# Optimization experiments

Hardware: AMD Instinct MI355X
Metric: run time of the kernel (lower is better)

## Reference

```python
import jax, jax.numpy as jnp
import numpy as np

L = 32768
D_MODEL = 1024
D_HIDDEN = 1024


def setup_inputs() -> dict:
    key = jax.random.key(0)
    k_in, k_lam, k_B, k_C, k_D = jax.random.split(key, 5)
    inputs = jax.random.normal(k_in, (L, D_MODEL), dtype=jnp.float32)
    # uniform_init(normalization=sqrt(d_model)): U(-1,1)/sqrt(d_model) -> |lambda|<1, stable recurrence
    diag_lambda = jax.random.uniform(k_lam, (D_HIDDEN,), dtype=jnp.float32, minval=-1.0, maxval=1.0) / jnp.sqrt(float(D_MODEL))
    B = jax.random.normal(k_B, (D_HIDDEN, D_MODEL), dtype=jnp.float32) / jnp.sqrt(float(D_MODEL))
    C = jax.random.normal(k_C, (D_MODEL, D_HIDDEN), dtype=jnp.float32) / jnp.sqrt(float(D_HIDDEN))
    D = jax.random.normal(k_D, (D_MODEL,), dtype=jnp.float32)
    return {"inputs": inputs, "diag_lambda": diag_lambda, "B": B, "C": C, "D": D}


def _binop_diag(q_i, q_j):
    # elementwise diagonal linear-recurrence combine: (A, b) o (A', b') = (A'*A, A'*b + b')
    A_i, b_i = q_i
    A_j, b_j = q_j
    return (A_j * A_i, A_j * b_i + b_j)


def reference(inputs, diag_lambda, B, C, D):
    # h_t = lambda * h_{t-1} + B x_t ; y_t = C h_t + D * x_t
    Bu = jnp.einsum('ld,hd->lh', inputs, B)                     # [L, d_hidden]
    Lam = jnp.broadcast_to(diag_lambda[None, :], Bu.shape)      # [L, d_hidden]
    _, hidden = jax.lax.associative_scan(_binop_diag, (Lam, Bu))
    outputs = jnp.einsum('lh,dh->ld', hidden, C) + D[None, :] * inputs
    return outputs
```

## Files before the change

### kernel.cpp

```cpp
#include <hip/hip_runtime.h>

#define L_SEQ   32768
#define DMODEL  1024
#define DHIDDEN 1024
#define CHS     64
#define NCHS    (L_SEQ / CHS)
#define HALO    12

using f32x4  = __attribute__((ext_vector_type(4))) float;
using bf16x8 = __attribute__((ext_vector_type(8))) short;

typedef __attribute__((address_space(3))) unsigned char lds_byte_t;
typedef __attribute__((address_space(1))) const unsigned char glb_byte_t;

__device__ __forceinline__ void gld_lds16(const void* g, void* l) {
    __builtin_amdgcn_global_load_lds((glb_byte_t*)g, (lds_byte_t*)l, 16, 0, 0);
}

__device__ __forceinline__ unsigned short f2bf(float x) {
    unsigned u = __float_as_uint(x);
    unsigned r = u + 0x7fffu + ((u >> 16) & 1u);
    return (unsigned short)(r >> 16);
}
__device__ __forceinline__ float bf2f(unsigned short h) {
    return __uint_as_float(((unsigned)h) << 16);
}
__device__ __forceinline__ void split2(float x, unsigned short& hi, unsigned short& lo) {
    hi = f2bf(x);
    lo = f2bf(x - bf2f(hi));
}

__global__ __launch_bounds__(256)
void split_kernel(const float* __restrict__ in, unsigned short* __restrict__ hi,
                  unsigned short* __restrict__ lo, int n4)
{
    int i = blockIdx.x * 256 + threadIdx.x;
    const int stride = gridDim.x * 256;
    for (; i < n4; i += stride) {
        float4 v = ((const float4*)in)[i];
        ushort4 h, l;
        split2(v.x, h.x, l.x);
        split2(v.y, h.y, l.y);
        split2(v.z, h.z, l.z);
        split2(v.w, h.w, l.w);
        ((ushort4*)hi)[i] = h;
        ((ushort4*)lo)[i] = l;
    }
}

template<int EPI>
__global__ __launch_bounds__(256, 2)
void gemm3_bt(const unsigned short* __restrict__ Ahi, const unsigned short* __restrict__ Alo,
              const unsigned short* __restrict__ Bthi, const unsigned short* __restrict__ Btlo,
              int M, int N, int K,
              float* __restrict__ outF,
              const float* __restrict__ Dv, const float* __restrict__ X)
{
    __shared__ __align__(16) unsigned short smem[2][16384];

    const int tid  = threadIdx.x;
    const int wave = tid >> 6;
    const int lane = tid & 63;

    const int nbn = N >> 7;
    const int nwg = gridDim.x;
    const int cpx = nwg >> 3;
    const int swz = (blockIdx.x & 7) * cpx + (blockIdx.x >> 3);
    const int bm = swz / nbn, bn = swz % nbn;
    const int m0 = bm << 7, n0 = bn << 7;

    const int wr = wave >> 1, wc = wave & 1;

    const unsigned short* plane = (wave == 0) ? Ahi : (wave == 1) ? Alo
                                 : (wave == 2) ? Bthi : Btlo;
    const int r0 = (wave < 2) ? m0 : n0;

    const unsigned short* src0; const unsigned short* src1;
    const unsigned short* src2; const unsigned short* src3;
    const unsigned short* src4; const unsigned short* src5;
    const unsigned short* src6; const unsigned short* src7;
    int lo0, lo1, lo2, lo3, lo4, lo5, lo6, lo7;
    {
        const unsigned short* sp[8];
        int lofs[8];
#pragma unroll
        for (int i = 0; i < 8; ++i) {
            const int c   = i * 64 + lane;
            const int kg  = c >> 7;
            const int row = c & 127;
            sp[i]   = plane + (size_t)(r0 + row) * K + kg * 8;
            lofs[i] = wave * 4096 + c * 8;
        }
        src0 = sp[0]; src1 = sp[1]; src2 = sp[2]; src3 = sp[3];
        src4 = sp[4]; src5 = sp[5]; src6 = sp[6]; src7 = sp[7];
        lo0 = lofs[0]; lo1 = lofs[1]; lo2 = lofs[2]; lo3 = lofs[3];
        lo4 = lofs[4]; lo5 = lofs[5]; lo6 = lofs[6]; lo7 = lofs[7];
    }

#define STAGE(BUF, KOFF)                                                    \
    do {                                                                    \
        gld_lds16(src0 + (KOFF), &smem[BUF][lo0]);                          \
        gld_lds16(src1 + (KOFF), &smem[BUF][lo1]);                          \
        gld_lds16(src2 + (KOFF), &smem[BUF][lo2]);                          \
        gld_lds16(src3 + (KOFF), &smem[BUF][lo3]);                          \
        gld_lds16(src4 + (KOFF), &smem[BUF][lo4]);                          \
        gld_lds16(src5 + (KOFF), &smem[BUF][lo5]);                          \
        gld_lds16(src6 + (KOFF), &smem[BUF][lo6]);                          \
        gld_lds16(src7 + (KOFF), &smem[BUF][lo7]);                          \
    } while (0)

    f32x4 acc[4][4] = {};
    const int kgL = lane >> 4;
    const int rL  = lane & 15;

#define COMPUTE(BUF)                                                        \
    do {                                                                    \
        const unsigned short* sc = smem[BUF];                               \
        bf16x8 ah[4], al[4], bh[4], bl[4];                                  \
        _Pragma("unroll")                                                   \
        for (int mi = 0; mi < 4; ++mi) {                                    \
            const int off = kgL * 1024 + (wr * 64 + mi * 16 + rL) * 8;      \
            ah[mi] = *(const bf16x8*)&sc[off];                              \
            al[mi] = *(const bf16x8*)&sc[4096 + off];                       \
        }                                                                   \
        _Pragma("unroll")                                                   \
        for (int ni = 0; ni < 4; ++ni) {                                    \
            const int off = kgL * 1024 + (wc * 64 + ni * 16 + rL) * 8;      \
            bh[ni] = *(const bf16x8*)&sc[8192 + off];                       \
            bl[ni] = *(const bf16x8*)&sc[12288 + off];                      \
        }                                                                   \
        _Pragma("unroll")                                                   \
        for (int mi = 0; mi < 4; ++mi)                                      \
            _Pragma("unroll")                                               \
            for (int ni = 0; ni < 4; ++ni) {                                \
                acc[mi][ni] = __builtin_amdgcn_mfma_f32_16x16x32_bf16(      \
                    ah[mi], bh[ni], acc[mi][ni], 0, 0, 0);                  \
                acc[mi][ni] = __builtin_amdgcn_mfma_f32_16x16x32_bf16(      \
                    ah[mi], bl[ni], acc[mi][ni], 0, 0, 0);                  \
                acc[mi][ni] = __builtin_amdgcn_mfma_f32_16x16x32_bf16(      \
                    al[mi], bh[ni], acc[mi][ni], 0, 0, 0);                  \
            }                                                               \
    } while (0)

    STAGE(0, 0);
    __syncthreads();

    for (int k0 = 0; k0 < K; k0 += 64) {
        STAGE(1, k0 + 32);
        COMPUTE(0);
        __syncthreads();
        if (k0 + 64 < K) STAGE(0, k0 + 64);
        COMPUTE(1);
        __syncthreads();
    }
#undef STAGE
#undef COMPUTE

    const int orow = (lane >> 4) * 4;
    const int ocol = lane & 15;
#pragma unroll
    for (int mi = 0; mi < 4; ++mi)
#pragma unroll
        for (int ni = 0; ni < 4; ++ni)
#pragma unroll
            for (int r = 0; r < 4; ++r) {
                const int row = m0 + wr * 64 + mi * 16 + orow + r;
                const int col = n0 + wc * 64 + ni * 16 + ocol;
                float v = acc[mi][ni][r];
                if (EPI)
                    v = fmaf(Dv[col], X[(size_t)row * N + col], v);
                outF[(size_t)row * N + col] = v;
            }
}

__global__ __launch_bounds__(256)
void scan_fused(const float* __restrict__ Bu, const float* __restrict__ lam,
                unsigned short* __restrict__ Hhi, unsigned short* __restrict__ Hlo)
{
    const int c  = blockIdx.x;
    const int h0 = threadIdx.x * 4;
    float4 l4 = *(const float4*)&lam[h0];
    float hx = 0.f, hy = 0.f, hz = 0.f, hw = 0.f;

    const int r0 = c * CHS;
    const int hs = (c == 0) ? 0 : HALO;
    const float* p = Bu + (size_t)(r0 - hs) * DHIDDEN + h0;

    for (int r = 0; r < hs; ++r) {
        float4 v = *(const float4*)p;
        hx = fmaf(l4.x, hx, v.x);
        hy = fmaf(l4.y, hy, v.y);
        hz = fmaf(l4.z, hz, v.z);
        hw = fmaf(l4.w, hw, v.w);
        p += DHIDDEN;
    }

    unsigned short* ph = Hhi + (size_t)r0 * DHIDDEN + h0;
    unsigned short* pl = Hlo + (size_t)r0 * DHIDDEN + h0;
    for (int r = 0; r < CHS; ++r) {
        float4 v = *(const float4*)p;
        hx = fmaf(l4.x, hx, v.x);
        hy = fmaf(l4.y, hy, v.y);
        hz = fmaf(l4.z, hz, v.z);
        hw = fmaf(l4.w, hw, v.w);
        ushort4 oh, ol;
        split2(hx, oh.x, ol.x);
        split2(hy, oh.y, ol.y);
        split2(hz, oh.z, ol.z);
        split2(hw, oh.w, ol.w);
        *(ushort4*)ph = oh;
        *(ushort4*)pl = ol;
        p  += DHIDDEN;
        ph += DHIDDEN;
        pl += DHIDDEN;
    }
}

extern "C" void kernel_launch(void* const* d_in, const int* in_sizes, int n_in,
                              void* d_out, int out_size, void* d_ws, size_t ws_size,
                              hipStream_t stream)
{
    const float* X   = (const float*)d_in[0];
    const float* lam = (const float*)d_in[1];
    const float* B   = (const float*)d_in[2];
    const float* C   = (const float*)d_in[3];
    const float* Dv  = (const float*)d_in[4];
    float* out = (float*)d_out;

    unsigned short* Xhi = (unsigned short*)d_out;
    unsigned short* Xlo = Xhi + (size_t)L_SEQ * DMODEL;

    float* Bu = (float*)d_ws;
    unsigned short* Hhi = (unsigned short*)(Bu + (size_t)L_SEQ * DHIDDEN);
    unsigned short* Hlo = Hhi + (size_t)L_SEQ * DHIDDEN;
    unsigned short* Bhi = Hlo + (size_t)L_SEQ * DHIDDEN;
    unsigned short* Blo = Bhi + (size_t)DHIDDEN * DMODEL;
    unsigned short* Chi = Blo + (size_t)DHIDDEN * DMODEL;
    unsigned short* Clo = Chi + (size_t)DMODEL * DHIDDEN;

    dim3 blk(256);

    split_kernel<<<dim3(2048), blk, 0, stream>>>(X, Xhi, Xlo, (L_SEQ * DMODEL) / 4);
    split_kernel<<<dim3(1024), blk, 0, stream>>>(B, Bhi, Blo, (DHIDDEN * DMODEL) / 4);
    split_kernel<<<dim3(1024), blk, 0, stream>>>(C, Chi, Clo, (DMODEL * DHIDDEN) / 4);

    gemm3_bt<0><<<dim3((L_SEQ / 128) * (DHIDDEN / 128)), blk, 0, stream>>>(
        Xhi, Xlo, Bhi, Blo, L_SEQ, DHIDDEN, DMODEL, Bu, nullptr, nullptr);

    scan_fused<<<dim3(NCHS), blk, 0, stream>>>(Bu, lam, Hhi, Hlo);

    gemm3_bt<1><<<dim3((L_SEQ / 128) * (DMODEL / 128)), blk, 0, stream>>>(
        Hhi, Hlo, Chi, Clo, L_SEQ, DMODEL, DHIDDEN, out, Dv, X);
}
```

Before: 1.388 ms.

## Use partial vmcnt waits with raw barriers to overlap next stage loads with MFMA

Replaces __syncthreads in the double-buffered GEMM main loop with explicit s_waitcnt vmcnt(8) plus s_barrier. The next stage's global-to-LDS loads can then stay in flight while the current buffer is computed. The loop is unrolled to a fixed 15 iterations plus a peeled tail that drains with vmcnt(0). This hardcodes K=1024 and assumes each STAGE issues exactly 8 loads per thread; if that count is wrong, a race is possible.

```diff
diff --git a/kernel.cpp b/kernel.cpp
--- a/kernel.cpp
+++ b/kernel.cpp
@@ -142,19 +142,49 @@
             }                                                               \
     } while (0)
 
+#define PHASE_SYNC_8()                                                      \
+    do {                                                                    \
+        asm volatile("s_waitcnt vmcnt(8)" ::: "memory");                    \
+        __builtin_amdgcn_s_barrier();                                       \
+        __builtin_amdgcn_sched_barrier(0);                                  \
+    } while (0)
+#define PHASE_SYNC_0()                                                      \
+    do {                                                                    \
+        asm volatile("s_waitcnt vmcnt(0)" ::: "memory");                    \
+        __builtin_amdgcn_s_barrier();                                       \
+        __builtin_amdgcn_sched_barrier(0);                                  \
+    } while (0)
+#define END_BARRIER()                                                       \
+    do {                                                                    \
+        __builtin_amdgcn_s_barrier();                                       \
+        __builtin_amdgcn_sched_barrier(0);                                  \
+    } while (0)
+
     STAGE(0, 0);
-    __syncthreads();
-
-    for (int k0 = 0; k0 < K; k0 += 64) {
+
+    for (int it = 0; it < 15; ++it) {
+        const int k0 = it * 64;
         STAGE(1, k0 + 32);
+        PHASE_SYNC_8();
         COMPUTE(0);
-        __syncthreads();
-        if (k0 + 64 < K) STAGE(0, k0 + 64);
+        END_BARRIER();
+        STAGE(0, k0 + 64);
+        PHASE_SYNC_8();
         COMPUTE(1);
-        __syncthreads();
-    }
+        END_BARRIER();
+    }
+    STAGE(1, 992);
+    PHASE_SYNC_8();
+    COMPUTE(0);
+    END_BARRIER();
+    PHASE_SYNC_0();
+    COMPUTE(1);
+
 #undef STAGE
 #undef COMPUTE
+#undef PHASE_SYNC_8
+#undef PHASE_SYNC_0
+#undef END_BARRIER
 
     const int orow = (lane >> 4) * 4;
     const int ocol = lane & 15;
```

Result: no change. 1.369 ms (-1.3%).
